# Kernel optimization log

Measured on AMD Instinct MI355X. Metric: run time of the kernel, lower is better.

## Reference

```python
import jax, jax.numpy as jnp
import numpy as np

B, T, N, H = 128, 512, 256, 1024  # batch, seq_len(input_size), num_nodes(params.input_size), hidden_size


def _glorot(k, shape):
    fan_in, fan_out = shape
    s = float(np.sqrt(6.0 / (fan_in + fan_out)))
    return jax.random.uniform(k, shape, minval=-s, maxval=s, dtype=jnp.float32)


def setup_inputs() -> dict:
    key = jax.random.key(0)
    ks = jax.random.split(key, 10)
    return {
        "x": jax.random.normal(ks[0], (B, T, N), dtype=jnp.float32),
        # SAGEConv 1: lin_l (neighbor mean, with bias), lin_r (root, no bias)
        "Wl1": _glorot(ks[1], (T, H)), "Wr1": _glorot(ks[2], (T, H)), "b1": jnp.zeros((H,), jnp.float32),
        # SAGEConv 2
        "Wl2": _glorot(ks[3], (H, H)), "Wr2": _glorot(ks[4], (H, H)), "b2": jnp.zeros((H,), jnp.float32),
        # block_1: Linear(H,H,bias=False), Linear(H,T,bias=False), Sigmoid
        "W1a": _glorot(ks[5], (H, H)), "W1b": _glorot(ks[6], (H, T)),
        # block_2: Linear(N,N,bias=False), Linear(N,H,bias=False), Sigmoid
        "W2a": _glorot(ks[7], (N, N)), "W2b": _glorot(ks[8], (N, H)),
    }


def _sage(h, Wl, Wr, b):
    # Dense graph without self-loops: mean over neighbors = (sum_all - self) / (n-1).
    n = h.shape[1]
    mean_nb = (jnp.sum(h, axis=1, keepdims=True) - h) / (n - 1)  # [B,N,F]
    return mean_nb @ Wl + h @ Wr + b  # SAGEConv: lin_l(aggr) + lin_r(x)


def reference(x, Wl1, Wr1, b1, Wl2, Wr2, b2, W1a, W1b, W2a, W2b):
    h = jnp.transpose(x, (0, 2, 1))            # [B,N,T] nodes=features
    h = _sage(h, Wl1, Wr1, b1)                 # [B,N,H]
    h = _sage(h, Wl2, Wr2, b2)                 # [B,N,H]
    h = jax.nn.sigmoid((h @ W1a) @ W1b)        # [B,N,T]
    h = jnp.transpose(h, (0, 2, 1))            # [B,T,N]
    return jax.nn.sigmoid((h @ W2a) @ W2b)     # [B,T,H]
```

## Files before the change

kernel.cpp:

```cpp
#include <hip/hip_runtime.h>
#include <hip/hip_bf16.h>

#define B_ 128
#define T_ 512
#define N_ 256
#define H_ 1024

typedef unsigned short u16;
typedef __attribute__((ext_vector_type(8))) __bf16 bf16x8;
typedef __attribute__((ext_vector_type(4))) float f32x4;

__device__ __forceinline__ u16 f2bf(float f) {
    unsigned u = __float_as_uint(f);
    u = (u + 0x7FFFu + ((u >> 16) & 1u)) >> 16;
    return (u16)u;
}

__device__ __forceinline__ void g2l16(const void* g, void* l) {
    __builtin_amdgcn_global_load_lds(
        (const __attribute__((address_space(1))) void*)g,
        (__attribute__((address_space(3))) void*)l,
        16, 0, 0);
}

#define ASLOT 12288u

#define GATE(N) { asm volatile("s_waitcnt vmcnt(" #N ")" ::: "memory"); \
                  __builtin_amdgcn_s_barrier(); }
#define LD4(dst, base) { _Pragma("unroll") for (int i_ = 0; i_ < 4; ++i_) \
    dst[i_] = *(const bf16x8*)(L + (base) + i_ * 512); }
#define STAGE(tile) { const u16* a_ = gA + (size_t)(tile) * 32; \
    const u16* b_ = gB + (size_t)(tile) * 32; \
    const unsigned s_ = (unsigned)(((tile) % 3) * ASLOT); \
    g2l16(a_, dA0 + s_);  g2l16(a_ + jstr, dA0 + s_ + 4096); \
    g2l16(b_, dB0 + s_); }
#define BODY(t) { \
    const unsigned sl = (unsigned)(((t) % 3) * ASLOT); \
    bf16x8 ra[4], rb[4]; \
    LD4(ra, sl + aoff); \
    LD4(rb, sl + boff); \
    if ((t) + 2 < nt) STAGE((t) + 2); \
    __builtin_amdgcn_s_setprio(1); \
    _Pragma("unroll") for (int mi_ = 0; mi_ < 4; ++mi_) \
    _Pragma("unroll") for (int ni_ = 0; ni_ < 4; ++ni_) \
        acc[mi_][ni_] = __builtin_amdgcn_mfma_f32_16x16x32_bf16( \
            ra[mi_], rb[ni_], acc[mi_][ni_], 0, 0, 0); \
    __builtin_amdgcn_s_setprio(0); }

template<int ACT, int OUT>
__global__ __launch_bounds__(512, 2) void gemm_e3(
    const u16* __restrict__ A, const u16* __restrict__ Bt,
    float* __restrict__ Cf, u16* __restrict__ Cb,
    const float* __restrict__ bias,
    int Nc, int K, int bshift, int gysh)
{
    __shared__ u16 L[36864];
    const int tid = threadIdx.x;
    const int wave = tid >> 6, lane = tid & 63;
    const int l16 = lane & 15, lh = lane >> 4;
    const int wm = wave >> 1, wn = wave & 1;

    const int qq = (int)gridDim.x >> 3;
    const int orig = (int)blockIdx.x;
    const int wg = (orig & 7) * qq + (orig >> 3);
    const int by = wg & ((1 << gysh) - 1), bx = wg >> gysh;
    const size_t m0 = (size_t)bx * 256, n0 = (size_t)by * 128;

    const int sx8 = (lh ^ ((l16 >> 1) & 3)) * 8;
    const unsigned aoff = (unsigned)(wm * 2048 + l16 * 32 + sx8);
    const unsigned boff = (unsigned)(8192 + wn * 2048 + l16 * 32 + sx8);

    const int srow = tid >> 2;
    const int sslot = (tid & 3) ^ ((srow >> 1) & 3);
    const size_t jstr = (size_t)128 * K;
    const u16* gA = A + (m0 + srow) * (size_t)K + sslot * 8;
    const u16* gB = Bt + (n0 + srow) * (size_t)K + sslot * 8;
    u16* const dA0 = L + (unsigned)(wave * 512);
    u16* const dB0 = L + 8192 + (unsigned)(wave * 512);

    f32x4 acc[4][4] = {};
    const int nt = K >> 5;

    STAGE(0); STAGE(1);
    for (int t = 0; t < nt - 1; ++t) {
        GATE(3);
        BODY(t);
    }
    GATE(0);
    { const int t = nt - 1; BODY(t); }

    const size_t NcS = (size_t)Nc;
#pragma unroll
    for (int mi = 0; mi < 4; ++mi) {
#pragma unroll
        for (int ni = 0; ni < 4; ++ni) {
            size_t rbase = m0 + wm * 64 + mi * 16 + lh * 4;
            size_t col   = n0 + wn * 64 + ni * 16 + l16;
            if (OUT == 2) {
                u16 e[4];
#pragma unroll
                for (int rr = 0; rr < 4; ++rr) {
                    float v = acc[mi][ni][rr];
                    v = 1.0f / (1.0f + __expf(-v));
                    e[rr] = f2bf(v);
                }
                size_t qi = ((rbase >> 8) * (size_t)T_ + col) * N_ + (rbase & 255);
                *(uint2*)(Cb + qi) = *(const uint2*)e;
            } else {
#pragma unroll
                for (int rr = 0; rr < 4; ++rr) {
                    size_t row = rbase + rr;
                    float v = acc[mi][ni][rr];
                    if (bias) v += bias[(row >> bshift) * NcS + col];
                    if (ACT) v = 1.0f / (1.0f + __expf(-v));
                    if (OUT == 1) Cf[row * NcS + col] = v;
                    else          Cb[row * NcS + col] = f2bf(v);
                }
            }
        }
    }
}

__device__ __forceinline__ void small_body(
    const u16* __restrict__ A, const u16* __restrict__ Bt,
    float* __restrict__ Cf, u16* __restrict__ Cb,
    const float* __restrict__ bias,
    int Nc, int K, int lda, int ldb, int outmode, int bshift,
    float kscale, float bmul, int bx, int by)
{
    __shared__ u16 lA[128 * 64];
    __shared__ u16 lB[128 * 64];
    const int tid = threadIdx.x;
    const int wave = tid >> 6, lane = tid & 63;
    const int l16 = lane & 15, lh = lane >> 4;
    const int wm = wave >> 1, wn = wave & 1;
    const long m0 = (long)bx * 128;
    const long n0 = (long)by * 128;

    f32x4 acc[4][4] = {};

    for (int k0 = 0; k0 < K; k0 += 64) {
#pragma unroll
        for (int j = 0; j < 4; ++j) {
            int c = j * 256 + tid;
            int row = c >> 3, col = (c & 7) << 3;
            g2l16(A  + (m0 + row) * (size_t)lda + k0 + col, &lA[(size_t)(j * 256 + (wave << 6)) * 8]);
            g2l16(Bt + (n0 + row) * (size_t)ldb + k0 + col, &lB[(size_t)(j * 256 + (wave << 6)) * 8]);
        }
        __syncthreads();
#pragma unroll
        for (int s = 0; s < 2; ++s) {
            bf16x8 af[4], bfr[4];
#pragma unroll
            for (int mi = 0; mi < 4; ++mi)
                af[mi] = *(const bf16x8*)&lA[((wm << 6) + (mi << 4) + l16) * 64 + s * 32 + (lh << 3)];
#pragma unroll
            for (int ni = 0; ni < 4; ++ni)
                bfr[ni] = *(const bf16x8*)&lB[((wn << 6) + (ni << 4) + l16) * 64 + s * 32 + (lh << 3)];
#pragma unroll
            for (int mi = 0; mi < 4; ++mi)
#pragma unroll
                for (int ni = 0; ni < 4; ++ni)
                    acc[mi][ni] = __builtin_amdgcn_mfma_f32_16x16x32_bf16(af[mi], bfr[ni], acc[mi][ni], 0, 0, 0);
        }
        __syncthreads();
    }

#pragma unroll
    for (int mi = 0; mi < 4; ++mi) {
#pragma unroll
        for (int ni = 0; ni < 4; ++ni) {
            long rbase = m0 + (wm << 6) + (mi << 4) + (lh << 2);
            long col   = n0 + (wn << 6) + (ni << 4) + l16;
#pragma unroll
            for (int r = 0; r < 4; ++r) {
                long row = rbase + r;
                float v = acc[mi][ni][r] * kscale;
                if (outmode == 2) {
                    v += (col < 1024 ? 1.0f : 256.0f / 255.0f) * bias[col & 1023];
                    Cb[(size_t)row * Nc + col] = f2bf(v);
                } else {
                    if (bias) v += bmul * bias[(size_t)(row >> bshift) * Nc + col];
                    if (outmode == 1) Cf[(size_t)row * Nc + col] = v;
                    else              Cb[(size_t)row * Nc + col] = f2bf(v);
                }
            }
        }
    }
}

template<int OUTF32>
__global__ __launch_bounds__(256) void gemm_bt(
    const u16* __restrict__ A, const u16* __restrict__ Bt,
    float* __restrict__ Cf, u16* __restrict__ Cb,
    const float* __restrict__ bias,
    int Nc, int K, int bshift, float kscale, float bmul)
{
    small_body(A, Bt, Cf, Cb, bias, Nc, K, K, K, OUTF32, bshift, kscale, bmul,
               blockIdx.x, blockIdx.y);
}

__global__ __launch_bounds__(256) void k_small4(
    const u16* __restrict__ W2cat, const u16* __restrict__ W1rm, u16* __restrict__ W12t,
    const u16* __restrict__ W1bt, const u16* __restrict__ W1ab, u16* __restrict__ W1ct,
    const u16* __restrict__ W2bt, const u16* __restrict__ W2ab, u16* __restrict__ W2ct,
    const u16* __restrict__ s1b, const u16* __restrict__ Wcat, u16* __restrict__ Acat,
    const float* __restrict__ b1)
{
    const int bid = blockIdx.x;
    if (bid < 32) {
        small_body(W2cat, W1rm, nullptr, W12t, nullptr, 512, 1024, 2048, 1024,
                   0, 0, 1.0f, 0.0f, bid >> 2, bid & 3);
    } else if (bid < 64) {
        int r = bid - 32;
        small_body(W1bt, W1ab, nullptr, W1ct, nullptr, 1024, 1024, 1024, 1024,
                   0, 0, 1.0f, 0.0f, r >> 3, r & 7);
    } else if (bid < 80) {
        int r = bid - 64;
        small_body(W2bt, W2ab, nullptr, W2ct, nullptr, 256, 256, 256, 256,
                   0, 0, 1.0f, 0.0f, r >> 1, r & 1);
    } else {
        int r = bid - 80;
        small_body(s1b, Wcat, nullptr, Acat, b1, 2048, 512, 512, 512,
                   2, 0, 1.0f / 255.0f, 0.0f, 0, r);
    }
}

__global__ __launch_bounds__(256) void k_trx_rs(
    const float* __restrict__ x, u16* __restrict__ h, u16* __restrict__ s1b)
{
    __shared__ float sm[32][257];
    const int b = blockIdx.y, t0 = blockIdx.x * 32;
    const int tid = threadIdx.x;
    const float* xb = x + ((size_t)b * T_ + t0) * N_;
#pragma unroll 8
    for (int j = 0; j < 32; ++j)
        sm[j][tid] = xb[(size_t)j * N_ + tid];
    __syncthreads();
    const int wave = tid >> 6, lane = tid & 63;
#pragma unroll
    for (int i = 0; i < 8; ++i) {
        int j = wave * 8 + i;
        float s = sm[j][lane] + sm[j][lane + 64] + sm[j][lane + 128] + sm[j][lane + 192];
#pragma unroll
        for (int o = 32; o; o >>= 1) s += __shfl_down(s, o, 64);
        if (lane == 0) s1b[(size_t)b * T_ + t0 + j] = f2bf(s);
    }
    u16 e[32];
#pragma unroll
    for (int j = 0; j < 32; ++j) e[j] = f2bf(sm[j][tid]);
    uint4* dst = (uint4*)(h + ((size_t)b * N_ + tid) * T_ + t0);
    const uint4* src = (const uint4*)e;
#pragma unroll
    for (int v = 0; v < 4; ++v) dst[v] = src[v];
}

__global__ void k_wtr(const float* __restrict__ Wl1, const float* __restrict__ Wr1,
                      const float* __restrict__ Wl2, const float* __restrict__ Wr2,
                      const float* __restrict__ W1b, const float* __restrict__ W2b,
                      const float* __restrict__ W1a, const float* __restrict__ W2a,
                      u16* __restrict__ Wcat, u16* __restrict__ W1rm,
                      u16* __restrict__ W2cat,
                      u16* __restrict__ W1bt, u16* __restrict__ W2bt,
                      u16* __restrict__ W1ab, u16* __restrict__ W2ab)
{
    __shared__ float tl[32][33], tr[32][33];
    int bid = blockIdx.x;
    const int tx = threadIdx.x, ty = threadIdx.y;
    if (bid < 512) {
        int r0 = (bid >> 5) * 32, c0 = (bid & 31) * 32;
#pragma unroll
        for (int i = 0; i < 4; ++i) {
            int r = r0 + ty + 8 * i;
            float wl = Wl1[(size_t)r * H_ + c0 + tx];
            float wr = Wr1[(size_t)r * H_ + c0 + tx];
            tl[ty + 8 * i][tx] = wl;
            tr[ty + 8 * i][tx] = wl + wr;
            W1rm[(size_t)r * H_ + c0 + tx] = f2bf(wr - wl * (1.0f / 255.0f));
        }
        __syncthreads();
#pragma unroll
        for (int i = 0; i < 4; ++i) {
            size_t o = (size_t)(c0 + ty + 8 * i) * T_ + r0 + tx;
            Wcat[o]                     = f2bf(tl[tx][ty + 8 * i]);
            Wcat[o + (size_t)1024 * T_] = f2bf(tr[tx][ty + 8 * i]);
        }
    } else if (bid < 1536) {
        bid -= 512;
        int r0 = (bid >> 5) * 32, c0 = (bid & 31) * 32;
#pragma unroll
        for (int i = 0; i < 4; ++i) {
            int r = r0 + ty + 8 * i;
            float wl = Wl2[(size_t)r * H_ + c0 + tx];
            float wr = Wr2[(size_t)r * H_ + c0 + tx];
            tl[ty + 8 * i][tx] = wr - wl * (1.0f / 255.0f);
            tr[ty + 8 * i][tx] = wl;
        }
        __syncthreads();
#pragma unroll
        for (int i = 0; i < 4; ++i) {
            size_t o = (size_t)(c0 + ty + 8 * i) * 2048 + r0 + tx;
            W2cat[o]        = f2bf(tl[tx][ty + 8 * i]);
            W2cat[o + 1024] = f2bf(tr[tx][ty + 8 * i]);
        }
    } else if (bid < 2048) {
        bid -= 1536;
        int r0 = (bid >> 4) * 32, c0 = (bid & 15) * 32;
#pragma unroll
        for (int i = 0; i < 4; ++i)
            tl[ty + 8 * i][tx] = W1b[(size_t)(r0 + ty + 8 * i) * T_ + c0 + tx];
        __syncthreads();
#pragma unroll
        for (int i = 0; i < 4; ++i)
            W1bt[(size_t)(c0 + ty + 8 * i) * H_ + r0 + tx] = f2bf(tl[tx][ty + 8 * i]);
    } else if (bid < 2304) {
        bid -= 2048;
        int r0 = (bid >> 5) * 32, c0 = (bid & 31) * 32;
#pragma unroll
        for (int i = 0; i < 4; ++i)
            tl[ty + 8 * i][tx] = W2b[(size_t)(r0 + ty + 8 * i) * H_ + c0 + tx];
        __syncthreads();
#pragma unroll
        for (int i = 0; i < 4; ++i)
            W2bt[(size_t)(c0 + ty + 8 * i) * N_ + r0 + tx] = f2bf(tl[tx][ty + 8 * i]);
    } else {
        int i = (bid - 2304) * 256 + ty * 32 + tx;
        const int n1 = H_ * H_ / 8;
        const float* s; u16* d;
        if (i < n1) { s = W1a; d = W1ab; }
        else        { s = W2a; d = W2ab; i -= n1; }
        float4 a = ((const float4*)s)[2 * i], b = ((const float4*)s)[2 * i + 1];
        u16 e[8] = {f2bf(a.x), f2bf(a.y), f2bf(a.z), f2bf(a.w),
                    f2bf(b.x), f2bf(b.y), f2bf(b.z), f2bf(b.w)};
        ((uint4*)d)[i] = *(const uint4*)e;
    }
}

extern "C" void kernel_launch(void* const* d_in, const int* in_sizes, int n_in,
                              void* d_out, int out_size, void* d_ws, size_t ws_size,
                              hipStream_t stream)
{
    const float* x   = (const float*)d_in[0];
    const float* Wl1 = (const float*)d_in[1];
    const float* Wr1 = (const float*)d_in[2];
    const float* b1  = (const float*)d_in[3];
    const float* Wl2 = (const float*)d_in[4];
    const float* Wr2 = (const float*)d_in[5];
    const float* b2  = (const float*)d_in[6];
    const float* W1a = (const float*)d_in[7];
    const float* W1b = (const float*)d_in[8];
    const float* W2a = (const float*)d_in[9];
    const float* W2b = (const float*)d_in[10];
    float* out = (float*)d_out;

    char* ws = (char*)d_ws;
    size_t off = 0;
    auto alloc = [&](size_t bytes) -> char* {
        char* p = ws + off;
        off += (bytes + 255) & ~(size_t)255;
        return p;
    };

    const size_t BN = (size_t)B_ * N_;
    const size_t BT = (size_t)B_ * T_;

    u16* h_bf   = (u16*)alloc(BN * T_ * 2);
    u16* h2_bf  = (u16*)alloc(BN * H_ * 2);
    u16* Wcat   = (u16*)alloc((size_t)2048 * T_ * 2);
    u16* W1rm   = (u16*)alloc((size_t)T_ * H_ * 2);
    u16* W2cat  = (u16*)alloc((size_t)H_ * 2048 * 2);
    u16* W1bt   = (u16*)alloc((size_t)T_ * H_ * 2);
    u16* W1ab   = (u16*)alloc((size_t)H_ * H_ * 2);
    u16* W1ct   = (u16*)alloc((size_t)T_ * H_ * 2);
    u16* W2bt   = (u16*)alloc((size_t)H_ * N_ * 2);
    u16* W2ab   = (u16*)alloc((size_t)N_ * N_ * 2);
    u16* W2ct   = (u16*)alloc((size_t)H_ * N_ * 2);
    u16* W12t   = (u16*)alloc((size_t)H_ * T_ * 2);
    u16* s1b    = (u16*)alloc(BT * 2);
    u16* Acat   = (u16*)alloc((size_t)B_ * 2048 * 2);
    float* t12  = (float*)alloc((size_t)B_ * H_ * 4);

    u16* q_bf = h_bf;

    k_wtr<<<dim3(2848), dim3(32, 8), 0, stream>>>(Wl1, Wr1, Wl2, Wr2, W1b, W2b, W1a, W2a,
                                                  Wcat, W1rm, W2cat, W1bt, W2bt, W1ab, W2ab);
    k_trx_rs<<<dim3(T_ / 32, B_), 256, 0, stream>>>(x, h_bf, s1b);
    k_small4<<<dim3(96), 256, 0, stream>>>(W2cat, W1rm, W12t, W1bt, W1ab, W1ct,
                                           W2bt, W2ab, W2ct, s1b, Wcat, Acat, b1);
    gemm_bt<1><<<dim3(1, H_ / 128), 256, 0, stream>>>(Acat, W2cat, t12, nullptr, b2,
                                                      H_, 2048, 31, 1.0f, 1.0f);

    gemm_e3<0, 0><<<dim3(1024), 512, 0, stream>>>(h_bf, W12t, nullptr, h2_bf, t12, H_, T_, 8, 3);
    gemm_e3<1, 2><<<dim3(512), 512, 0, stream>>>(h2_bf, W1ct, nullptr, q_bf, nullptr, T_, H_, 0, 2);
    gemm_e3<1, 1><<<dim3(2048), 512, 0, stream>>>(q_bf, W2ct, out, nullptr, nullptr, H_, N_, 0, 3);
}
```

Before: 291.6 us.

## Use 4-wave 256-thread blocks with 64x128 per-wave tiles in main GEMMs

Reworks the GEMM kernel from 8 waves, each computing a 64x64 tile, to 4 waves, each computing 64x128 of the same 256x128 block tile. Each wave now loads a wider B fragment and issues 32 MFMAs per k-step. Each thread issues 6 global-to-LDS loads per stage, and the wait count is adjusted to match. This raises the MFMA-to-LDS-read ratio and cuts A-fragment reloads across waves, at the cost of doubled accumulator registers and fewer waves to hide latency.

Result: slower. 381.8 us (+31.0%).

```diff
diff --git a/kernel.cpp b/kernel.cpp
--- a/kernel.cpp
+++ b/kernel.cpp
@@ -32,23 +32,30 @@
 #define STAGE(tile) { const u16* a_ = gA + (size_t)(tile) * 32; \
     const u16* b_ = gB + (size_t)(tile) * 32; \
     const unsigned s_ = (unsigned)(((tile) % 3) * ASLOT); \
-    g2l16(a_, dA0 + s_);  g2l16(a_ + jstr, dA0 + s_ + 4096); \
-    g2l16(b_, dB0 + s_); }
+    g2l16(a_,            dA0 + s_); \
+    g2l16(a_ + rstr,     dA0 + s_ + 2048); \
+    g2l16(a_ + 2 * rstr, dA0 + s_ + 4096); \
+    g2l16(a_ + 3 * rstr, dA0 + s_ + 6144); \
+    g2l16(b_,            dB0 + s_); \
+    g2l16(b_ + rstr,     dB0 + s_ + 2048); }
 #define BODY(t) { \
     const unsigned sl = (unsigned)(((t) % 3) * ASLOT); \
-    bf16x8 ra[4], rb[4]; \
-    LD4(ra, sl + aoff); \
-    LD4(rb, sl + boff); \
+    bf16x8 ra[4], rb[4], rb2[4]; \
+    LD4(ra,  sl + aoff); \
+    LD4(rb,  sl + boff); \
+    LD4(rb2, sl + boff + 2048); \
     if ((t) + 2 < nt) STAGE((t) + 2); \
     __builtin_amdgcn_s_setprio(1); \
     _Pragma("unroll") for (int mi_ = 0; mi_ < 4; ++mi_) \
-    _Pragma("unroll") for (int ni_ = 0; ni_ < 4; ++ni_) \
-        acc[mi_][ni_] = __builtin_amdgcn_mfma_f32_16x16x32_bf16( \
-            ra[mi_], rb[ni_], acc[mi_][ni_], 0, 0, 0); \
+    _Pragma("unroll") for (int ni_ = 0; ni_ < 4; ++ni_) { \
+        acc[mi_][ni_]     = __builtin_amdgcn_mfma_f32_16x16x32_bf16( \
+            ra[mi_], rb[ni_],  acc[mi_][ni_],     0, 0, 0); \
+        acc[mi_][ni_ + 4] = __builtin_amdgcn_mfma_f32_16x16x32_bf16( \
+            ra[mi_], rb2[ni_], acc[mi_][ni_ + 4], 0, 0, 0); } \
     __builtin_amdgcn_s_setprio(0); }
 
 template<int ACT, int OUT>
-__global__ __launch_bounds__(512, 2) void gemm_e3(
+__global__ __launch_bounds__(256, 2) void gemm_w4(
     const u16* __restrict__ A, const u16* __restrict__ Bt,
     float* __restrict__ Cf, u16* __restrict__ Cb,
     const float* __restrict__ bias,
@@ -58,7 +65,6 @@
     const int tid = threadIdx.x;
     const int wave = tid >> 6, lane = tid & 63;
     const int l16 = lane & 15, lh = lane >> 4;
-    const int wm = wave >> 1, wn = wave & 1;
 
     const int qq = (int)gridDim.x >> 3;
     const int orig = (int)blockIdx.x;
@@ -67,23 +73,23 @@
     const size_t m0 = (size_t)bx * 256, n0 = (size_t)by * 128;
 
     const int sx8 = (lh ^ ((l16 >> 1) & 3)) * 8;
-    const unsigned aoff = (unsigned)(wm * 2048 + l16 * 32 + sx8);
-    const unsigned boff = (unsigned)(8192 + wn * 2048 + l16 * 32 + sx8);
+    const unsigned aoff = (unsigned)(wave * 2048 + l16 * 32 + sx8);
+    const unsigned boff = (unsigned)(8192 + l16 * 32 + sx8);
 
     const int srow = tid >> 2;
     const int sslot = (tid & 3) ^ ((srow >> 1) & 3);
-    const size_t jstr = (size_t)128 * K;
+    const size_t rstr = (size_t)64 * K;
     const u16* gA = A + (m0 + srow) * (size_t)K + sslot * 8;
     const u16* gB = Bt + (n0 + srow) * (size_t)K + sslot * 8;
     u16* const dA0 = L + (unsigned)(wave * 512);
     u16* const dB0 = L + 8192 + (unsigned)(wave * 512);
 
-    f32x4 acc[4][4] = {};
+    f32x4 acc[4][8] = {};
     const int nt = K >> 5;
 
     STAGE(0); STAGE(1);
     for (int t = 0; t < nt - 1; ++t) {
-        GATE(3);
+        GATE(6);
         BODY(t);
     }
     GATE(0);
@@ -93,9 +99,9 @@
 #pragma unroll
     for (int mi = 0; mi < 4; ++mi) {
 #pragma unroll
-        for (int ni = 0; ni < 4; ++ni) {
-            size_t rbase = m0 + wm * 64 + mi * 16 + lh * 4;
-            size_t col   = n0 + wn * 64 + ni * 16 + l16;
+        for (int ni = 0; ni < 8; ++ni) {
+            size_t rbase = m0 + wave * 64 + mi * 16 + lh * 4;
+            size_t col   = n0 + ni * 16 + l16;
             if (OUT == 2) {
                 u16 e[4];
 #pragma unroll
@@ -390,7 +396,7 @@
     gemm_bt<1><<<dim3(1, H_ / 128), 256, 0, stream>>>(Acat, W2cat, t12, nullptr, b2,
                                                       H_, 2048, 31, 1.0f, 1.0f);
 
-    gemm_e3<0, 0><<<dim3(1024), 512, 0, stream>>>(h_bf, W12t, nullptr, h2_bf, t12, H_, T_, 8, 3);
-    gemm_e3<1, 2><<<dim3(512), 512, 0, stream>>>(h2_bf, W1ct, nullptr, q_bf, nullptr, T_, H_, 0, 2);
-    gemm_e3<1, 1><<<dim3(2048), 512, 0, stream>>>(q_bf, W2ct, out, nullptr, nullptr, H_, N_, 0, 3);
-}
+    gemm_w4<0, 0><<<dim3(1024), 256, 0, stream>>>(h_bf, W12t, nullptr, h2_bf, t12, H_, T_, 8, 3);
+    gemm_w4<1, 2><<<dim3(512), 256, 0, stream>>>(h2_bf, W1ct, nullptr, q_bf, nullptr, T_, H_, 0, 2);
+    gemm_w4<1, 1><<<dim3(2048), 256, 0, stream>>>(q_bf, W2ct, out, nullptr, nullptr, H_, N_, 0, 3);
+}
```
